# Optimization experiments

Measured on AMD Instinct MI355X. Metric: run time of the kernel, lower is better.

Reference implementation:

```python
import jax, jax.numpy as jnp
import numpy as np

B, S, D, H = 4, 2048, 1024, 16
DK = D // H


def setup_inputs() -> dict:
    key = jax.random.key(0)
    ks = jax.random.split(key, 11)
    inp = {
        'query': jax.random.normal(ks[0], (B, S, D), jnp.float32),
        'key': jax.random.normal(ks[1], (B, S, D), jnp.float32),
        'value': jax.random.normal(ks[2], (B, S, D), jnp.float32),
        'mask': jnp.tril(jnp.ones((1, 1, S, S), dtype=bool)),  # causal
    }
    sc = 1.0 / np.sqrt(D)
    inp['w_q'] = jax.random.normal(ks[3], (D, D), jnp.float32) * sc
    inp['b_q'] = jnp.zeros((D,), jnp.float32)
    inp['w_k'] = jax.random.normal(ks[4], (D, D), jnp.float32) * sc
    inp['b_k'] = jnp.zeros((D,), jnp.float32)
    inp['w_v'] = jax.random.normal(ks[5], (D, D), jnp.float32) * sc
    inp['b_v'] = jnp.zeros((D,), jnp.float32)
    inp['w_o'] = jax.random.normal(ks[6], (D, D), jnp.float32) * sc
    inp['b_o'] = jnp.zeros((D,), jnp.float32)
    return inp


def _split_heads(x):
    # Faithful to source: view(B, S, d_k, H) then permute(0,3,1,2)
    b, s, _ = x.shape
    return x.reshape(b, s, DK, H).transpose(0, 3, 1, 2)  # (B, H, S, DK)


def _concat_heads(x):
    # permute(0,2,1,3) -> reshape(B, S, d_k*H)
    b, h, s, dk = x.shape
    return x.transpose(0, 2, 1, 3).reshape(b, s, dk * h)


def reference(query, key, value, mask, w_q, b_q, w_k, b_k, w_v, b_v, w_o, b_o):
    q = query @ w_q.T + b_q
    k = key @ w_k.T + b_k
    v = value @ w_v.T + b_v
    q, k, v = _split_heads(q), _split_heads(k), _split_heads(v)
    scale = 1.0 / jnp.sqrt(jnp.asarray(DK, q.dtype))
    scores = jnp.einsum('bhqd,bhkd->bhqk', q, k) * scale
    scores = jnp.where(mask, scores, -jnp.inf)
    attn = jax.nn.softmax(scores, axis=-1)  # dropout p=0 -> identity
    out = jnp.einsum('bhqk,bhkd->bhqd', attn, v)
    return _concat_heads(out) @ w_o.T + b_o
```

## Files before the change

### kernel.cpp

```cpp
#include <hip/hip_runtime.h>

#define BB 4
#define SS 2048
#define DD 1024
#define HH 16
#define DK 64
#define MM (BB * SS)

typedef __bf16 bf16x8 __attribute__((ext_vector_type(8)));
typedef float f32x4 __attribute__((ext_vector_type(4)));
typedef unsigned short us8 __attribute__((ext_vector_type(8)));
typedef unsigned short us4 __attribute__((ext_vector_type(4)));

#define MFMA_BF16(a, b, c) __builtin_amdgcn_mfma_f32_16x16x32_bf16((a), (b), (c), 0, 0, 0)

__device__ __forceinline__ unsigned short f2bf(float f) {
  return __builtin_bit_cast(unsigned short, (__bf16)f);
}

__device__ __forceinline__ bf16x8 ld_frag(const unsigned short* p) {
  return __builtin_bit_cast(bf16x8, *(const us8*)p);
}

__device__ __forceinline__ void gl_lds16(const unsigned short* g, unsigned short* l) {
  __builtin_amdgcn_global_load_lds((const __attribute__((address_space(1))) void*)g,
                                   (__attribute__((address_space(3))) void*)l, 16, 0, 0);
}

__global__ void cvt_weights(const float* __restrict__ w0, const float* __restrict__ w1,
                            const float* __restrict__ w2, const float* __restrict__ w3,
                            unsigned short* __restrict__ dst) {
  const float* src = (blockIdx.y == 0) ? w0 : (blockIdx.y == 1) ? w1 : (blockIdx.y == 2) ? w2 : w3;
  unsigned short* d = dst + (size_t)blockIdx.y * (DD * DD);
  int idx = (blockIdx.x * 256 + threadIdx.x) * 4;
  float4 v = *(const float4*)(src + idx);
  us4 o;
  o[0] = f2bf(v.x); o[1] = f2bf(v.y); o[2] = f2bf(v.z); o[3] = f2bf(v.w);
  *(us4*)(d + idx) = o;
}

__global__ __launch_bounds__(256, 3) void qkv_gemm(
    const float* __restrict__ xq, const float* __restrict__ xk, const float* __restrict__ xv,
    const unsigned short* __restrict__ wb,
    const float* __restrict__ bq, const float* __restrict__ bk, const float* __restrict__ bv,
    unsigned short* __restrict__ qh, unsigned short* __restrict__ kh,
    unsigned short* __restrict__ vt) {
  const int mode = blockIdx.z;
  const float* x = (mode == 0) ? xq : (mode == 1) ? xk : xv;
  const unsigned short* w = wb + (size_t)mode * (DD * DD);
  const float* bias = (mode == 0) ? bq : (mode == 1) ? bk : bv;

  const int m0 = blockIdx.x * 128;
  const int h0 = blockIdx.y * 2;

  __shared__ unsigned short smem[17408];
  unsigned short* sA = smem;
  unsigned short* sB = smem + 8192;

  const int tid = threadIdx.x;
  const int lane = tid & 63;
  const int wave = tid >> 6;
  const int wm = wave & 1, wn = wave >> 1;
  const int quad = lane >> 4, l16 = lane & 15;

  f32x4 acc[4][4];
#pragma unroll
  for (int i = 0; i < 4; i++)
#pragma unroll
    for (int j = 0; j < 4; j++) acc[i][j] = f32x4{0.f, 0.f, 0.f, 0.f};

  const int arow = tid >> 1, ahalf = tid & 1;
  const float* ag = x + (size_t)(m0 + arow) * DD + ahalf * 32;
  unsigned short* arow_base = sA + ahalf * 4096 + arow * 32;
  const int asw = (arow >> 1) & 3;

  const unsigned short* bsrc[4];
  unsigned short* bdst[4];
#pragma unroll
  for (int j = 0; j < 4; j++) {
    int cid = tid + j * 256;
    int half = cid >> 9, rr = (cid & 511) >> 2, c8 = (cid & 3) << 3;
    int n = ((rr & 63) << 4) + h0 + (rr >> 6);
    bsrc[j] = w + (size_t)n * DD + half * 32 + c8;
    bdst[j] = sB + half * 4096 + rr * 32 + c8;
  }

  float4 va[8];
  us8 vbr[4];
#pragma unroll
  for (int i = 0; i < 8; i++) va[i] = *(const float4*)(ag + 0 + i * 4);
#pragma unroll
  for (int j = 0; j < 4; j++) vbr[j] = *(const us8*)(bsrc[j] + 0);

  for (int k0 = 0; k0 < DD; k0 += 64) {
    __syncthreads();
#pragma unroll
    for (int c = 0; c < 4; c++) {
      us8 o;
      o[0] = f2bf(va[2 * c].x); o[1] = f2bf(va[2 * c].y);
      o[2] = f2bf(va[2 * c].z); o[3] = f2bf(va[2 * c].w);
      o[4] = f2bf(va[2 * c + 1].x); o[5] = f2bf(va[2 * c + 1].y);
      o[6] = f2bf(va[2 * c + 1].z); o[7] = f2bf(va[2 * c + 1].w);
      *(us8*)(arow_base + ((c ^ asw) << 3)) = o;
    }
#pragma unroll
    for (int j = 0; j < 4; j++) *(us8*)(bdst[j]) = vbr[j];
    __syncthreads();

    if (k0 + 64 < DD) {
#pragma unroll
      for (int i = 0; i < 8; i++) va[i] = *(const float4*)(ag + k0 + 64 + i * 4);
#pragma unroll
      for (int j = 0; j < 4; j++) vbr[j] = *(const us8*)(bsrc[j] + k0 + 64);
    }

#pragma unroll
    for (int kk = 0; kk < 2; kk++) {
      bf16x8 af[4];
#pragma unroll
      for (int mi = 0; mi < 4; mi++) {
        int row = wm * 64 + mi * 16 + l16;
        af[mi] = ld_frag(sA + kk * 4096 + row * 32 + ((quad ^ ((row >> 1) & 3)) << 3));
      }
#pragma unroll
      for (int ni = 0; ni < 4; ni++) {
        bf16x8 bfr = ld_frag(sB + kk * 4096 + (wn * 64 + ni * 16 + l16) * 32 + quad * 8);
#pragma unroll
        for (int mi = 0; mi < 4; mi++) acc[mi][ni] = MFMA_BF16(af[mi], bfr, acc[mi][ni]);
      }
    }
  }

  if (mode < 2) {
    unsigned short* outp = (mode == 0) ? qh : kh;
#pragma unroll
    for (int mi = 0; mi < 4; mi++) {
#pragma unroll
      for (int ni = 0; ni < 4; ni++) {
        int c = wn * 64 + ni * 16 + l16;
        int h = h0 + (c >> 6), dk = c & 63;
        float bvv = bias[(dk << 4) + h];
        int mg0 = m0 + wm * 64 + mi * 16 + quad * 4;
#pragma unroll
        for (int r = 0; r < 4; r++) {
          int mg = mg0 + r;
          int bb = mg >> 11, s = mg & 2047;
          size_t dst = ((size_t)((bb << 4) + h) * SS + s) * DK + dk;
          outp[dst] = f2bf(acc[mi][ni][r] + bvv);
        }
      }
    }
  } else {
    __syncthreads();
#pragma unroll
    for (int mi = 0; mi < 4; mi++) {
#pragma unroll
      for (int ni = 0; ni < 4; ni++) {
        int c = wn * 64 + ni * 16 + l16;
        int h = h0 + (c >> 6), dk = c & 63;
        float bvv = bias[(dk << 4) + h];
        int ml0 = wm * 64 + mi * 16 + quad * 4;
#pragma unroll
        for (int r = 0; r < 4; r++)
          smem[c * 136 + ml0 + r] = f2bf(acc[mi][ni][r] + bvv);
      }
    }
    __syncthreads();
    int bb = m0 >> 11;
    int sbase = m0 & 2047;
#pragma unroll
    for (int i = 0; i < 8; i++) {
      int idx = tid + i * 256;
      int c = idx >> 4, mc = (idx & 15) << 3;
      int h = h0 + (c >> 6), dk = c & 63;
      size_t dst = ((size_t)((bb << 4) + h) * DK + dk) * SS + sbase + mc;
      *(us8*)(vt + dst) = *(const us8*)(smem + c * 136 + mc);
    }
  }
}

__global__ __launch_bounds__(256, 2) void attn(
    const unsigned short* __restrict__ qh, const unsigned short* __restrict__ kh,
    const unsigned short* __restrict__ vt, unsigned short* __restrict__ outc) {
  const int bh = blockIdx.x;
  const int by = blockIdx.y;
  const int b = bh >> 4, h = bh & 15;
  const unsigned short* Qp = qh + (size_t)bh * SS * DK;
  const unsigned short* Kp = kh + (size_t)bh * SS * DK;
  const unsigned short* Vp = vt + (size_t)bh * DK * SS;

  __shared__ unsigned short sK[128 * 72];
  __shared__ unsigned short sV[64 * 136];

  const int tid = threadIdx.x;
  const int lane = tid & 63;
  const int wave = tid >> 6;
  const int quad = lane >> 4, l16 = lane & 15;
  const int wq0 = wave * 32;

  const float sl = 0.125f * 1.44269504088896f;

  for (int pass = 0; pass < 2; pass++) {
    const int qt = pass ? (15 - by) : by;
    const int q0 = qt * 128;

    bf16x8 aq[2][2];
#pragma unroll
    for (int mi = 0; mi < 2; mi++)
#pragma unroll
      for (int kk = 0; kk < 2; kk++)
        aq[mi][kk] = ld_frag(Qp + (size_t)(q0 + wq0 + mi * 16 + l16) * DK + kk * 32 + quad * 8);

    f32x4 o_acc[2][4];
    float mrowL[2], lrowL[2];
#pragma unroll
    for (int mi = 0; mi < 2; mi++) {
#pragma unroll
      for (int ni = 0; ni < 4; ni++) o_acc[mi][ni] = f32x4{0.f, 0.f, 0.f, 0.f};
      mrowL[mi] = -1e30f;
      lrowL[mi] = 0.f;
    }

    for (int kt = 0; kt <= qt; kt++) {
      const int k0 = kt * 128;
      const bool diag = (kt == qt);
      __syncthreads();
#pragma unroll
      for (int i = 0; i < 4; i++) {
        int idx = tid + i * 256;
        int row = idx >> 3, c8 = (idx & 7) << 3;
        *(us8*)(sK + row * 72 + c8) = *(const us8*)(Kp + (size_t)(k0 + row) * DK + c8);
      }
#pragma unroll
      for (int i = 0; i < 4; i++) {
        int idx = tid + i * 256;
        int row = idx >> 4, cc = (idx & 15) << 3;
        *(us8*)(sV + row * 136 + cc) = *(const us8*)(Vp + (size_t)row * SS + k0 + cc);
      }
      __syncthreads();

      f32x4 sc[2][8];
#pragma unroll
      for (int mi = 0; mi < 2; mi++)
#pragma unroll
        for (int kti = 0; kti < 8; kti++) sc[mi][kti] = f32x4{0.f, 0.f, 0.f, 0.f};
#pragma unroll
      for (int kti = 0; kti < 8; kti++) {
#pragma unroll
        for (int kk = 0; kk < 2; kk++) {
          bf16x8 ak = ld_frag(sK + (kti * 16 + l16) * 72 + kk * 32 + quad * 8);
#pragma unroll
          for (int mi = 0; mi < 2; mi++) sc[mi][kti] = MFMA_BF16(ak, aq[mi][kk], sc[mi][kti]);
        }
      }

      if (diag) {
#pragma unroll
        for (int mi = 0; mi < 2; mi++) {
          int ql = wq0 + mi * 16 + l16;
#pragma unroll
          for (int kti = 0; kti < 8; kti++)
#pragma unroll
            for (int r = 0; r < 4; r++) {
              int kl = kti * 16 + quad * 4 + r;
              float v = sc[mi][kti][r] * sl;
              sc[mi][kti][r] = (kl > ql) ? -1e30f : v;
            }
        }
      } else {
#pragma unroll
        for (int mi = 0; mi < 2; mi++)
#pragma unroll
          for (int kti = 0; kti < 8; kti++)
#pragma unroll
            for (int r = 0; r < 4; r++) sc[mi][kti][r] *= sl;
      }

      float alphaL[2];
#pragma unroll
      for (int mi = 0; mi < 2; mi++) {
        f32x4 vm = sc[mi][0];
#pragma unroll
        for (int kti = 1; kti < 8; kti++)
#pragma unroll
          for (int r = 0; r < 4; r++) vm[r] = fmaxf(vm[r], sc[mi][kti][r]);
        float mx = fmaxf(fmaxf(vm[0], vm[1]), fmaxf(vm[2], vm[3]));
        mx = fmaxf(mx, __shfl_xor(mx, 16, 64));
        mx = fmaxf(mx, __shfl_xor(mx, 32, 64));
        float mnew = fmaxf(mrowL[mi], mx);
        alphaL[mi] = exp2f(mrowL[mi] - mnew);
        mrowL[mi] = mnew;
      }

#pragma unroll
      for (int mi = 0; mi < 2; mi++) {
#pragma unroll
        for (int r = 0; r < 4; r++) {
          float a = __shfl(alphaL[mi], quad * 4 + r, 64);
#pragma unroll
          for (int ni = 0; ni < 4; ni++) o_acc[mi][ni][r] *= a;
        }
        us4 pk[8];
        f32x4 vs = f32x4{0.f, 0.f, 0.f, 0.f};
#pragma unroll
        for (int kti = 0; kti < 8; kti++) {
#pragma unroll
          for (int r = 0; r < 4; r++) {
            float p = exp2f(sc[mi][kti][r] - mrowL[mi]);
            vs[r] += p;
            pk[kti][r] = f2bf(p);
          }
        }
        float ls = (vs[0] + vs[1]) + (vs[2] + vs[3]);
        ls += __shfl_xor(ls, 16, 64);
        ls += __shfl_xor(ls, 32, 64);
        lrowL[mi] = lrowL[mi] * alphaL[mi] + ls;

#pragma unroll
        for (int c = 0; c < 4; c++) {
          bf16x8 ap = __builtin_bit_cast(
              bf16x8, __builtin_shufflevector(pk[2 * c], pk[2 * c + 1], 0, 1, 2, 3, 4, 5, 6, 7));
#pragma unroll
          for (int ni = 0; ni < 4; ni++) {
            const unsigned short* vb = sV + (ni * 16 + l16) * 136 + c * 32 + quad * 4;
            us4 lo = *(const us4*)vb;
            us4 hi = *(const us4*)(vb + 16);
            bf16x8 bfr = __builtin_bit_cast(
                bf16x8, __builtin_shufflevector(lo, hi, 0, 1, 2, 3, 4, 5, 6, 7));
            o_acc[mi][ni] = MFMA_BF16(ap, bfr, o_acc[mi][ni]);
          }
        }
      }
    }

#pragma unroll
    for (int mi = 0; mi < 2; mi++) {
#pragma unroll
      for (int r = 0; r < 4; r++) {
        float lr = __shfl(lrowL[mi], quad * 4 + r, 64);
        float inv = 1.0f / lr;
        int qg = q0 + wq0 + mi * 16 + quad * 4 + r;
        size_t rowbase = ((size_t)(b * SS + qg)) * DD + h * DK;
#pragma unroll
        for (int ni = 0; ni < 4; ni++) {
          int dk = ni * 16 + l16;
          outc[rowbase + dk] = f2bf(o_acc[mi][ni][r] * inv);
        }
      }
    }
    __syncthreads();
  }
}

__global__ __launch_bounds__(256, 4) void out_proj(
    const unsigned short* __restrict__ ac, const unsigned short* __restrict__ wo,
    const float* __restrict__ bias, float* __restrict__ out) {
  const int m0 = blockIdx.x * 128;
  const int n0 = blockIdx.y * 128;
  __shared__ unsigned short sA[8192];
  __shared__ unsigned short sB[8192];

  const int tid = threadIdx.x;
  const int lane = tid & 63;
  const int wave = tid >> 6;
  const int wm = wave & 1, wn = wave >> 1;
  const int quad = lane >> 4, l16 = lane & 15;

  f32x4 acc[4][4];
#pragma unroll
  for (int i = 0; i < 4; i++)
#pragma unroll
    for (int j = 0; j < 4; j++) acc[i][j] = f32x4{0.f, 0.f, 0.f, 0.f};

  for (int k0 = 0; k0 < DD; k0 += 64) {
    __syncthreads();
#pragma unroll
    for (int j = 0; j < 4; j++) {
      int cid = tid + j * 256;
      int half = cid >> 9;
      int rr = (cid & 511) >> 2;
      int c8 = (cid & 3) << 3;
      gl_lds16(ac + (size_t)(m0 + rr) * DD + k0 + half * 32 + c8,
               sA + half * 4096 + rr * 32 + c8);
    }
#pragma unroll
    for (int j = 0; j < 4; j++) {
      int cid = tid + j * 256;
      int half = cid >> 9;
      int rr = (cid & 511) >> 2;
      int c8 = (cid & 3) << 3;
      gl_lds16(wo + (size_t)(n0 + rr) * DD + k0 + half * 32 + c8,
               sB + half * 4096 + rr * 32 + c8);
    }
    __syncthreads();
#pragma unroll
    for (int kk = 0; kk < 2; kk++) {
      bf16x8 af[4];
#pragma unroll
      for (int mi = 0; mi < 4; mi++)
        af[mi] = ld_frag(sA + kk * 4096 + (wm * 64 + mi * 16 + l16) * 32 + quad * 8);
#pragma unroll
      for (int ni = 0; ni < 4; ni++) {
        bf16x8 bfr = ld_frag(sB + kk * 4096 + (wn * 64 + ni * 16 + l16) * 32 + quad * 8);
#pragma unroll
        for (int mi = 0; mi < 4; mi++) acc[mi][ni] = MFMA_BF16(af[mi], bfr, acc[mi][ni]);
      }
    }
  }

#pragma unroll
  for (int mi = 0; mi < 4; mi++) {
#pragma unroll
    for (int ni = 0; ni < 4; ni++) {
      int n = n0 + wn * 64 + ni * 16 + l16;
      float bvv = bias[n];
      int mg0 = m0 + wm * 64 + mi * 16 + quad * 4;
#pragma unroll
      for (int r = 0; r < 4; r++) out[(size_t)(mg0 + r) * DD + n] = acc[mi][ni][r] + bvv;
    }
  }
}

extern "C" void kernel_launch(void* const* d_in, const int* in_sizes, int n_in,
                              void* d_out, int out_size, void* d_ws, size_t ws_size,
                              hipStream_t stream) {
  const float* q_in = (const float*)d_in[0];
  const float* k_in = (const float*)d_in[1];
  const float* v_in = (const float*)d_in[2];
  const float* w_q = (const float*)d_in[4];
  const float* b_q = (const float*)d_in[5];
  const float* w_k = (const float*)d_in[6];
  const float* b_k = (const float*)d_in[7];
  const float* w_v = (const float*)d_in[8];
  const float* b_v = (const float*)d_in[9];
  const float* w_o = (const float*)d_in[10];
  const float* b_o = (const float*)d_in[11];
  float* out = (float*)d_out;

  unsigned short* ws = (unsigned short*)d_ws;
  unsigned short* wb = ws;
  unsigned short* qh = ws + (size_t)4 * 1024 * 1024;
  unsigned short* kh = ws + (size_t)12 * 1024 * 1024;
  unsigned short* vt = ws + (size_t)20 * 1024 * 1024;
  unsigned short* outc = ws + (size_t)28 * 1024 * 1024;

  const size_t WSZ = (size_t)DD * DD;

  cvt_weights<<<dim3(1024, 4), 256, 0, stream>>>(w_q, w_k, w_v, w_o, wb);
  qkv_gemm<<<dim3(64, 8, 3), 256, 0, stream>>>(q_in, k_in, v_in, wb, b_q, b_k, b_v, qh, kh, vt);
  attn<<<dim3(64, 8), 256, 0, stream>>>(qh, kh, vt, outc);
  out_proj<<<dim3(64, 8), 256, 0, stream>>>(outc, wb + 3 * WSZ, b_o, out);
}
```

Before: 370.8 us.

## Drop LDS staging in QKV and output GEMMs, load MFMA fragments directly

Both projection GEMMs stop staging tiles through shared memory with barriers. Each lane now loads its MFMA fragments straight from global memory, converting fp32 to bf16 in registers for the QKV inputs. The V-transpose epilogue now writes 4-element vectors directly instead of going through an LDS transpose. This removes syncthreads and LDS traffic, but tiles are no longer shared across waves, so each wave reloads the same operand rows and relies on L1/L2 for reuse. It also changes the occupancy hint.

```diff
diff --git a/kernel.cpp b/kernel.cpp
--- a/kernel.cpp
+++ b/kernel.cpp
@@ -20,11 +20,6 @@
 
 __device__ __forceinline__ bf16x8 ld_frag(const unsigned short* p) {
   return __builtin_bit_cast(bf16x8, *(const us8*)p);
-}
-
-__device__ __forceinline__ void gl_lds16(const unsigned short* g, unsigned short* l) {
-  __builtin_amdgcn_global_load_lds((const __attribute__((address_space(1))) void*)g,
-                                   (__attribute__((address_space(3))) void*)l, 16, 0, 0);
 }
 
 __global__ void cvt_weights(const float* __restrict__ w0, const float* __restrict__ w1,
@@ -53,82 +48,48 @@
   const int m0 = blockIdx.x * 128;
   const int h0 = blockIdx.y * 2;
 
-  __shared__ unsigned short smem[17408];
-  unsigned short* sA = smem;
-  unsigned short* sB = smem + 8192;
-
   const int tid = threadIdx.x;
   const int lane = tid & 63;
   const int wave = tid >> 6;
   const int wm = wave & 1, wn = wave >> 1;
   const int quad = lane >> 4, l16 = lane & 15;
 
+  const float* aB[4];
+#pragma unroll
+  for (int mi = 0; mi < 4; mi++)
+    aB[mi] = x + (size_t)(m0 + wm * 64 + mi * 16 + l16) * DD + quad * 8;
+  const unsigned short* bB[4];
+#pragma unroll
+  for (int ni = 0; ni < 4; ni++) {
+    int c = wn * 64 + ni * 16 + l16;
+    int n = ((c & 63) << 4) + h0 + (c >> 6);
+    bB[ni] = w + (size_t)n * DD + quad * 8;
+  }
+
   f32x4 acc[4][4];
 #pragma unroll
   for (int i = 0; i < 4; i++)
 #pragma unroll
     for (int j = 0; j < 4; j++) acc[i][j] = f32x4{0.f, 0.f, 0.f, 0.f};
 
-  const int arow = tid >> 1, ahalf = tid & 1;
-  const float* ag = x + (size_t)(m0 + arow) * DD + ahalf * 32;
-  unsigned short* arow_base = sA + ahalf * 4096 + arow * 32;
-  const int asw = (arow >> 1) & 3;
-
-  const unsigned short* bsrc[4];
-  unsigned short* bdst[4];
-#pragma unroll
-  for (int j = 0; j < 4; j++) {
-    int cid = tid + j * 256;
-    int half = cid >> 9, rr = (cid & 511) >> 2, c8 = (cid & 3) << 3;
-    int n = ((rr & 63) << 4) + h0 + (rr >> 6);
-    bsrc[j] = w + (size_t)n * DD + half * 32 + c8;
-    bdst[j] = sB + half * 4096 + rr * 32 + c8;
-  }
-
-  float4 va[8];
-  us8 vbr[4];
-#pragma unroll
-  for (int i = 0; i < 8; i++) va[i] = *(const float4*)(ag + 0 + i * 4);
-#pragma unroll
-  for (int j = 0; j < 4; j++) vbr[j] = *(const us8*)(bsrc[j] + 0);
-
-  for (int k0 = 0; k0 < DD; k0 += 64) {
-    __syncthreads();
-#pragma unroll
-    for (int c = 0; c < 4; c++) {
+#pragma unroll 2
+  for (int k0 = 0; k0 < DD; k0 += 32) {
+    bf16x8 af[4], bfr[4];
+#pragma unroll
+    for (int mi = 0; mi < 4; mi++) {
+      float4 lo = *(const float4*)(aB[mi] + k0);
+      float4 hi = *(const float4*)(aB[mi] + k0 + 4);
       us8 o;
-      o[0] = f2bf(va[2 * c].x); o[1] = f2bf(va[2 * c].y);
-      o[2] = f2bf(va[2 * c].z); o[3] = f2bf(va[2 * c].w);
-      o[4] = f2bf(va[2 * c + 1].x); o[5] = f2bf(va[2 * c + 1].y);
-      o[6] = f2bf(va[2 * c + 1].z); o[7] = f2bf(va[2 * c + 1].w);
-      *(us8*)(arow_base + ((c ^ asw) << 3)) = o;
-    }
-#pragma unroll
-    for (int j = 0; j < 4; j++) *(us8*)(bdst[j]) = vbr[j];
-    __syncthreads();
-
-    if (k0 + 64 < DD) {
-#pragma unroll
-      for (int i = 0; i < 8; i++) va[i] = *(const float4*)(ag + k0 + 64 + i * 4);
-#pragma unroll
-      for (int j = 0; j < 4; j++) vbr[j] = *(const us8*)(bsrc[j] + k0 + 64);
-    }
-
-#pragma unroll
-    for (int kk = 0; kk < 2; kk++) {
-      bf16x8 af[4];
-#pragma unroll
-      for (int mi = 0; mi < 4; mi++) {
-        int row = wm * 64 + mi * 16 + l16;
-        af[mi] = ld_frag(sA + kk * 4096 + row * 32 + ((quad ^ ((row >> 1) & 3)) << 3));
-      }
-#pragma unroll
-      for (int ni = 0; ni < 4; ni++) {
-        bf16x8 bfr = ld_frag(sB + kk * 4096 + (wn * 64 + ni * 16 + l16) * 32 + quad * 8);
-#pragma unroll
-        for (int mi = 0; mi < 4; mi++) acc[mi][ni] = MFMA_BF16(af[mi], bfr, acc[mi][ni]);
-      }
-    }
+      o[0] = f2bf(lo.x); o[1] = f2bf(lo.y); o[2] = f2bf(lo.z); o[3] = f2bf(lo.w);
+      o[4] = f2bf(hi.x); o[5] = f2bf(hi.y); o[6] = f2bf(hi.z); o[7] = f2bf(hi.w);
+      af[mi] = __builtin_bit_cast(bf16x8, o);
+    }
+#pragma unroll
+    for (int ni = 0; ni < 4; ni++) bfr[ni] = ld_frag(bB[ni] + k0);
+#pragma unroll
+    for (int ni = 0; ni < 4; ni++)
+#pragma unroll
+      for (int mi = 0; mi < 4; mi++) acc[mi][ni] = MFMA_BF16(af[mi], bfr[ni], acc[mi][ni]);
   }
 
   if (mode < 2) {
@@ -151,7 +112,7 @@
       }
     }
   } else {
-    __syncthreads();
+    int bb = m0 >> 11;
 #pragma unroll
     for (int mi = 0; mi < 4; mi++) {
 #pragma unroll
@@ -159,22 +120,14 @@
         int c = wn * 64 + ni * 16 + l16;
         int h = h0 + (c >> 6), dk = c & 63;
         float bvv = bias[(dk << 4) + h];
-        int ml0 = wm * 64 + mi * 16 + quad * 4;
-#pragma unroll
-        for (int r = 0; r < 4; r++)
-          smem[c * 136 + ml0 + r] = f2bf(acc[mi][ni][r] + bvv);
-      }
-    }
-    __syncthreads();
-    int bb = m0 >> 11;
-    int sbase = m0 & 2047;
-#pragma unroll
-    for (int i = 0; i < 8; i++) {
-      int idx = tid + i * 256;
-      int c = idx >> 4, mc = (idx & 15) << 3;
-      int h = h0 + (c >> 6), dk = c & 63;
-      size_t dst = ((size_t)((bb << 4) + h) * DK + dk) * SS + sbase + mc;
-      *(us8*)(vt + dst) = *(const us8*)(smem + c * 136 + mc);
+        int mg0 = m0 + wm * 64 + mi * 16 + quad * 4;
+        int sbase = mg0 & 2047;
+        us4 o;
+#pragma unroll
+        for (int r = 0; r < 4; r++) o[r] = f2bf(acc[mi][ni][r] + bvv);
+        size_t dst = ((size_t)((bb << 4) + h) * DK + dk) * SS + sbase;
+        *(us4*)(vt + dst) = o;
+      }
     }
   }
 }
@@ -352,13 +305,11 @@
   }
 }
 
-__global__ __launch_bounds__(256, 4) void out_proj(
+__global__ __launch_bounds__(256, 3) void out_proj(
     const unsigned short* __restrict__ ac, const unsigned short* __restrict__ wo,
     const float* __restrict__ bias, float* __restrict__ out) {
   const int m0 = blockIdx.x * 128;
   const int n0 = blockIdx.y * 128;
-  __shared__ unsigned short sA[8192];
-  __shared__ unsigned short sB[8192];
 
   const int tid = threadIdx.x;
   const int lane = tid & 63;
@@ -366,46 +317,31 @@
   const int wm = wave & 1, wn = wave >> 1;
   const int quad = lane >> 4, l16 = lane & 15;
 
+  const unsigned short* aB[4];
+  const unsigned short* bB[4];
+#pragma unroll
+  for (int i = 0; i < 4; i++) {
+    aB[i] = ac + (size_t)(m0 + wm * 64 + i * 16 + l16) * DD + quad * 8;
+    bB[i] = wo + (size_t)(n0 + wn * 64 + i * 16 + l16) * DD + quad * 8;
+  }
+
   f32x4 acc[4][4];
 #pragma unroll
   for (int i = 0; i < 4; i++)
 #pragma unroll
     for (int j = 0; j < 4; j++) acc[i][j] = f32x4{0.f, 0.f, 0.f, 0.f};
 
-  for (int k0 = 0; k0 < DD; k0 += 64) {
-    __syncthreads();
-#pragma unroll
-    for (int j = 0; j < 4; j++) {
-      int cid = tid + j * 256;
-      int half = cid >> 9;
-      int rr = (cid & 511) >> 2;
-      int c8 = (cid & 3) << 3;
-      gl_lds16(ac + (size_t)(m0 + rr) * DD + k0 + half * 32 + c8,
-               sA + half * 4096 + rr * 32 + c8);
-    }
-#pragma unroll
-    for (int j = 0; j < 4; j++) {
-      int cid = tid + j * 256;
-      int half = cid >> 9;
-      int rr = (cid & 511) >> 2;
-      int c8 = (cid & 3) << 3;
-      gl_lds16(wo + (size_t)(n0 + rr) * DD + k0 + half * 32 + c8,
-               sB + half * 4096 + rr * 32 + c8);
-    }
-    __syncthreads();
-#pragma unroll
-    for (int kk = 0; kk < 2; kk++) {
-      bf16x8 af[4];
-#pragma unroll
-      for (int mi = 0; mi < 4; mi++)
-        af[mi] = ld_frag(sA + kk * 4096 + (wm * 64 + mi * 16 + l16) * 32 + quad * 8);
-#pragma unroll
-      for (int ni = 0; ni < 4; ni++) {
-        bf16x8 bfr = ld_frag(sB + kk * 4096 + (wn * 64 + ni * 16 + l16) * 32 + quad * 8);
-#pragma unroll
-        for (int mi = 0; mi < 4; mi++) acc[mi][ni] = MFMA_BF16(af[mi], bfr, acc[mi][ni]);
-      }
-    }
+#pragma unroll 2
+  for (int k0 = 0; k0 < DD; k0 += 32) {
+    bf16x8 af[4], bfr[4];
+#pragma unroll
+    for (int mi = 0; mi < 4; mi++) af[mi] = ld_frag(aB[mi] + k0);
+#pragma unroll
+    for (int ni = 0; ni < 4; ni++) bfr[ni] = ld_frag(bB[ni] + k0);
+#pragma unroll
+    for (int ni = 0; ni < 4; ni++)
+#pragma unroll
+      for (int mi = 0; mi < 4; mi++) acc[mi][ni] = MFMA_BF16(af[mi], bfr[ni], acc[mi][ni]);
   }
 
 #pragma unroll
```

Result: slower. 559.7 us (+50.9%).
